# Kernel tuning notes

Hardware: AMD Instinct MI355X
Metric: run time of the kernel (lower is better)

The kernel has to match this reference:

```python
import jax, jax.numpy as jnp
import numpy as np
import math

B, N, D, H, K = 32, 512, 768, 12, 8  # batch, patches, hidden_dim, heads, n_topic_groups
HD = D // H


def setup_inputs() -> dict:
    key = jax.random.key(0)
    ks = jax.random.split(key, 12)
    hidden_states = jax.random.normal(ks[0], (B, N, D), jnp.float32)
    # group ids in 1..K, every group present (required by original sorted-dict indexing)
    tid = jax.random.permutation(ks[1], (jnp.arange(B, dtype=jnp.int64) % K) + 1)
    s = 1.0 / math.sqrt(D)
    def lin(k):
        kw, kb = jax.random.split(k)
        return (jax.random.normal(kw, (D, D), jnp.float32) * s,
                jax.random.normal(kb, (D,), jnp.float32) * s)
    Wq, bq = lin(ks[2])
    Wk, bk = lin(ks[3])
    Wv, bv = lin(ks[4])
    Wo, bo = lin(ks[5])
    Wc, bc = lin(ks[6])  # Conv1d(D, D, kernel_size=1) == pointwise linear
    return dict(hidden_states=hidden_states, tid=tid, Wq=Wq, bq=bq, Wk=Wk, bk=bk,
                Wv=Wv, bv=bv, Wo=Wo, bo=bo, Wc=Wc, bc=bc)


def reference(hidden_states, tid, Wq, bq, Wk, bk, Wv, bv, Wo, bo, Wc, bc):
    # --- context(): per-group context_aware + mean, scattered back ---
    # context_aware(x) = mean over group of (x + conv1x1(x)); conv is pointwise so
    # it commutes with grouping -> compute per-sample then segment-mean.
    y = hidden_states + jnp.einsum('bnd,ed->bne', hidden_states, Wc) + bc  # [B,N,D]
    seg = tid - 1  # ids are 1..K
    sums = jax.ops.segment_sum(y, seg, num_segments=K)                      # [K,N,D]
    counts = jax.ops.segment_sum(jnp.ones((B,), y.dtype), seg, num_segments=K)
    means = sums / jnp.maximum(counts, 1.0)[:, None, None]
    contexts = means[seg] + hidden_states                                   # [B,N,D]

    # --- dual-stage attention (dropout rate 0 / eval mode) ---
    def heads(x):  # [B,N,D] -> [B,H,N,HD]
        return x.reshape(B, N, H, HD).transpose(0, 2, 1, 3)

    q = heads(hidden_states @ Wq.T + bq)
    t = heads(contexts @ Wq.T + bq)  # topic_states also passes through self.query
    k = heads(hidden_states @ Wk.T + bk)
    v = heads(hidden_states @ Wv.T + bv)

    scale = 1.0 / math.sqrt(HD)
    p1 = jax.nn.softmax(jnp.einsum('bhqd,bhkd->bhqk', t, k) * scale, axis=-1)
    v_t = jnp.einsum('bhqk,bhkd->bhqd', p1, v)
    p2 = jax.nn.softmax(jnp.einsum('bhqd,bhkd->bhqk', q, t) * scale, axis=-1)
    ctx = jnp.einsum('bhqk,bhkd->bhqd', p2, v_t)

    ctx = ctx.transpose(0, 2, 1, 3).reshape(B, N, D)
    return ctx @ Wo.T + bo
```

## Files before the change

kernel.cpp:

```cpp
#include <hip/hip_runtime.h>
#include <hip/hip_bf16.h>


typedef __bf16 bf16_t;
typedef __bf16 bf16x8 __attribute__((ext_vector_type(8)));
typedef __bf16 bf16x4 __attribute__((ext_vector_type(4)));
typedef float f32x4 __attribute__((ext_vector_type(4)));

#define B_ 32
#define N_ 512
#define D_ 768
#define H_ 12
#define HD_ 64
#define K_ 8
#define ND_ (N_ * D_)

__device__ __forceinline__ f32x4 mfma16(bf16x8 a, bf16x8 b, f32x4 c) {
  return __builtin_amdgcn_mfma_f32_16x16x32_bf16(a, b, c, 0, 0, 0);
}

__device__ __forceinline__ bf16x8 addv8(bf16x8 a, bf16x8 b) {
  bf16x8 o;
#pragma unroll
  for (int j = 0; j < 8; ++j) o[j] = (bf16_t)((float)a[j] + (float)b[j]);
  return o;
}

__device__ __forceinline__ int seg_of(const int* tid, int b) {
  const bool is64 = (tid[1] == 0);
  int v = is64 ? (int)((const long long*)tid)[b] : tid[b];
  return v - 1;
}

__global__ __launch_bounds__(256) void k_cvt(const float* __restrict__ in,
                                             bf16_t* __restrict__ out) {
  const size_t i = ((size_t)blockIdx.x * 256 + threadIdx.x) * 8;
  f32x4 a = *(const f32x4*)(in + i);
  f32x4 b = *(const f32x4*)(in + i + 4);
  bf16x8 o;
#pragma unroll
  for (int j = 0; j < 4; ++j) { o[j] = (bf16_t)a[j]; o[4 + j] = (bf16_t)b[j]; }
  *(bf16x8*)(out + i) = o;
}

__device__ __forceinline__ void gemm_core(const bf16_t* __restrict__ A,
                                          const bf16_t* __restrict__ Bw,
                                          char* smem, f32x4 (&acc)[4][4]) {
  const int t = threadIdx.x;
  const int lane = t & 63, w = t >> 6;
  const int quad = lane >> 4, l15 = lane & 15;
  const int r0 = t >> 2;
  const int c0e = (t & 3) * 8;
  const int mRow = (w >> 1) * 64, nCol = (w & 1) * 64;

  bf16x8 pa0 = *(const bf16x8*)(A + (size_t)r0 * D_ + c0e);
  bf16x8 pa1 = *(const bf16x8*)(A + (size_t)(r0 + 64) * D_ + c0e);
  bf16x8 pb0 = *(const bf16x8*)(Bw + (size_t)r0 * D_ + c0e);
  bf16x8 pb1 = *(const bf16x8*)(Bw + (size_t)(r0 + 64) * D_ + c0e);
  *(bf16x8*)(smem + t * 16) = pa0;
  *(bf16x8*)(smem + t * 16 + 4096) = pa1;
  *(bf16x8*)(smem + 8192 + t * 16) = pb0;
  *(bf16x8*)(smem + 8192 + t * 16 + 4096) = pb1;

  for (int kb = 0; kb < 24; ++kb) {
    __syncthreads();
    char* cur = smem + (kb & 1) * 16384;
    char* nxt = smem + ((kb + 1) & 1) * 16384;
    if (kb < 23) {
      const int k0 = (kb + 1) * 32;
      pa0 = *(const bf16x8*)(A + (size_t)r0 * D_ + k0 + c0e);
      pa1 = *(const bf16x8*)(A + (size_t)(r0 + 64) * D_ + k0 + c0e);
      pb0 = *(const bf16x8*)(Bw + (size_t)r0 * D_ + k0 + c0e);
      pb1 = *(const bf16x8*)(Bw + (size_t)(r0 + 64) * D_ + k0 + c0e);
    }
    bf16x8 af[4], bfr[4];
#pragma unroll
    for (int mt = 0; mt < 4; ++mt)
      af[mt] = *(const bf16x8*)(cur + (mRow + mt * 16 + l15) * 64 + quad * 16);
#pragma unroll
    for (int nt = 0; nt < 4; ++nt)
      bfr[nt] = *(const bf16x8*)(cur + 8192 + (nCol + nt * 16 + l15) * 64 +
                                 quad * 16);
#pragma unroll
    for (int mt = 0; mt < 4; ++mt)
#pragma unroll
      for (int nt = 0; nt < 4; ++nt)
        acc[mt][nt] = mfma16(af[mt], bfr[nt], acc[mt][nt]);
    if (kb < 23) {
      *(bf16x8*)(nxt + t * 16) = pa0;
      *(bf16x8*)(nxt + t * 16 + 4096) = pa1;
      *(bf16x8*)(nxt + 8192 + t * 16) = pb0;
      *(bf16x8*)(nxt + 8192 + t * 16 + 4096) = pb1;
    }
  }
}

__device__ __forceinline__ void zero_acc(f32x4 (&acc)[4][4]) {
  const f32x4 z = {0.f, 0.f, 0.f, 0.f};
#pragma unroll
  for (int a = 0; a < 4; ++a)
#pragma unroll
    for (int b = 0; b < 4; ++b) acc[a][b] = z;
}

__global__ __launch_bounds__(256) void k_gemm_qkv(
    const bf16_t* __restrict__ X, const bf16_t* __restrict__ Wq,
    const bf16_t* __restrict__ Wk, const bf16_t* __restrict__ Wv,
    const float* __restrict__ bq, const float* __restrict__ bk,
    const float* __restrict__ bv, bf16_t* __restrict__ Q,
    bf16_t* __restrict__ Kb, bf16_t* __restrict__ V) {
  __shared__ alignas(16) char smem[32768];
  const int wsel = blockIdx.x / 6, nb = blockIdx.x % 6;
  const bf16_t* W = wsel == 0 ? Wq : wsel == 1 ? Wk : Wv;
  const float* bias = wsel == 0 ? bq : wsel == 1 ? bk : bv;
  bf16_t* Out = wsel == 0 ? Q : wsel == 1 ? Kb : V;

  f32x4 acc[4][4];
  zero_acc(acc);
  gemm_core(X + (size_t)blockIdx.y * 128 * D_, W + (size_t)nb * 128 * D_, smem,
            acc);

  const int lane = threadIdx.x & 63, w = threadIdx.x >> 6;
  const int quad = lane >> 4, l15 = lane & 15;
  const int mbase = blockIdx.y * 128 + (w >> 1) * 64;
  const int nbase = nb * 128 + (w & 1) * 64;
#pragma unroll
  for (int nt = 0; nt < 4; ++nt) {
    const int col = nbase + nt * 16 + l15;
    const float bb = bias[col];
#pragma unroll
    for (int mt = 0; mt < 4; ++mt)
#pragma unroll
      for (int r = 0; r < 4; ++r) {
        const int row = mbase + mt * 16 + quad * 4 + r;
        Out[(size_t)row * D_ + col] = (bf16_t)(acc[mt][nt][r] + bb);
      }
  }
}

__global__ __launch_bounds__(256) void k_gemm_plain(
    const bf16_t* __restrict__ A, const bf16_t* __restrict__ W,
    const float* __restrict__ bias, const bf16_t* __restrict__ addA,
    void* __restrict__ Out, int outF32) {
  __shared__ alignas(16) char smem[32768];
  f32x4 acc[4][4];
  zero_acc(acc);
  gemm_core(A + (size_t)blockIdx.x * 128 * D_, W + (size_t)blockIdx.y * 128 * D_,
            smem, acc);
  const int lane = threadIdx.x & 63, w = threadIdx.x >> 6;
  const int quad = lane >> 4, l15 = lane & 15;
  const int mbase = blockIdx.x * 128 + (w >> 1) * 64;
  const int nbase = blockIdx.y * 128 + (w & 1) * 64;
#pragma unroll
  for (int nt = 0; nt < 4; ++nt) {
    const int col = nbase + nt * 16 + l15;
    const float bb = bias ? bias[col] : 0.f;
#pragma unroll
    for (int mt = 0; mt < 4; ++mt)
#pragma unroll
      for (int r = 0; r < 4; ++r) {
        const int row = mbase + mt * 16 + quad * 4 + r;
        float v = acc[mt][nt][r] + bb;
        if (addA) v += (float)addA[(size_t)row * D_ + col];
        const size_t oi = (size_t)row * D_ + col;
        if (outF32) ((float*)Out)[oi] = v;
        else ((bf16_t*)Out)[oi] = (bf16_t)v;
      }
  }
}

__global__ __launch_bounds__(256) void k_segmean(const float* __restrict__ X,
                                                 const int* __restrict__ tid,
                                                 bf16_t* __restrict__ M) {
  const size_t i = ((size_t)blockIdx.x * 256 + threadIdx.x) * 8;
  float acc[K_][8];
  float cnt[K_];
#pragma unroll
  for (int k = 0; k < K_; ++k) {
    cnt[k] = 0.f;
#pragma unroll
    for (int j = 0; j < 8; ++j) acc[k][j] = 0.f;
  }
  const bool is64 = (tid[1] == 0);
  for (int b = 0; b < B_; ++b) {
    const int s = (is64 ? (int)((const long long*)tid)[b] : tid[b]) - 1;
    const float* p = X + (size_t)b * ND_ + i;
    f32x4 y0 = *(const f32x4*)p;
    f32x4 y1 = *(const f32x4*)(p + 4);
#pragma unroll
    for (int k = 0; k < K_; ++k) {
      const float msk = (s == k) ? 1.f : 0.f;
      cnt[k] += msk;
#pragma unroll
      for (int j = 0; j < 4; ++j) {
        acc[k][j] += msk * y0[j];
        acc[k][4 + j] += msk * y1[j];
      }
    }
  }
#pragma unroll
  for (int k = 0; k < K_; ++k) {
    const float inv = 1.f / fmaxf(cnt[k], 1.f);
    bf16x8 o;
#pragma unroll
    for (int j = 0; j < 8; ++j) o[j] = (bf16_t)(acc[k][j] * inv);
    *(bf16x8*)(M + (size_t)k * ND_ + i) = o;
  }
}

__global__ __launch_bounds__(256) void k_attn(const bf16_t* __restrict__ Qp,
                                              const bf16_t* __restrict__ Kp,
                                              const bf16_t* __restrict__ Vp,
                                              const bf16_t* __restrict__ Madd,
                                              const int* __restrict__ tid,
                                              bf16_t* __restrict__ Op,
                                              int addq) {
  __shared__ alignas(16) __bf16 Kt[64][72];
  __shared__ alignas(16) __bf16 Vt[64][72];
  __shared__ alignas(16) __bf16 Pl[4][32][72];

  const int lane = threadIdx.x & 63, w = threadIdx.x >> 6;
  const int quad = lane >> 4, l15 = lane & 15;
  const int b = blockIdx.y / H_, h = blockIdx.y % H_;
  const int q0 = blockIdx.x * 128 + w * 32;
  const size_t base = (size_t)b * ND_ + h * HD_;
  const float C = 0.18033688011112042f;
  const int sg = seg_of(tid, b);
  const bf16_t* Mh = Madd + (size_t)sg * ND_ + h * HD_;

  bf16x8 aq[2][2];
#pragma unroll
  for (int mt = 0; mt < 2; ++mt)
#pragma unroll
    for (int ks = 0; ks < 2; ++ks) {
      const size_t off = (size_t)(q0 + mt * 16 + l15) * D_ + ks * 32 + quad * 8;
      bf16x8 q = *(const bf16x8*)(Qp + base + off);
      if (addq == 1) q = addv8(q, *(const bf16x8*)(Mh + off));
      aq[mt][ks] = q;
    }

  f32x4 O[2][4];
  float lacc[2][4];
  {
    const f32x4 z = {0.f, 0.f, 0.f, 0.f};
#pragma unroll
    for (int mt = 0; mt < 2; ++mt)
#pragma unroll
      for (int nt = 0; nt < 4; ++nt) O[mt][nt] = z;
#pragma unroll
    for (int mt = 0; mt < 2; ++mt)
#pragma unroll
      for (int r = 0; r < 4; ++r) lacc[mt][r] = 0.f;
  }

  const int sr = threadIdx.x >> 2, sc = threadIdx.x & 3;
  const int sig_sr = ((sr & 15) << 2) | (sr >> 4);

  bf16x8 kr[2], vr[2];
#pragma unroll
  for (int half = 0; half < 2; ++half) {
    const int cc = sc + half * 4;
    const size_t off = (size_t)sr * D_ + cc * 8;
    bf16x8 kv = *(const bf16x8*)(Kp + base + off);
    if (addq == 2) kv = addv8(kv, *(const bf16x8*)(Mh + off));
    kr[half] = kv;
    vr[half] = *(const bf16x8*)(Vp + base + off);
  }

  for (int c0 = 0; c0 < N_; c0 += 64) {
    __syncthreads();
#pragma unroll
    for (int half = 0; half < 2; ++half) {
      const int cc = sc + half * 4;
      *(bf16x8*)(&Kt[sr][cc * 8]) = kr[half];
#pragma unroll
      for (int j = 0; j < 8; ++j) Vt[cc * 8 + j][sig_sr] = vr[half][j];
    }
    __syncthreads();

    if (c0 + 64 < N_) {
#pragma unroll
      for (int half = 0; half < 2; ++half) {
        const int cc = sc + half * 4;
        const size_t off = (size_t)(c0 + 64 + sr) * D_ + cc * 8;
        bf16x8 kv = *(const bf16x8*)(Kp + base + off);
        if (addq == 2) kv = addv8(kv, *(const bf16x8*)(Mh + off));
        kr[half] = kv;
        vr[half] = *(const bf16x8*)(Vp + base + off);
      }
    }

    f32x4 S[2][4];
    {
      const f32x4 z = {0.f, 0.f, 0.f, 0.f};
#pragma unroll
      for (int mt = 0; mt < 2; ++mt)
#pragma unroll
        for (int nt = 0; nt < 4; ++nt) S[mt][nt] = z;
    }
#pragma unroll
    for (int ks = 0; ks < 2; ++ks) {
      bf16x8 bk[4];
#pragma unroll
      for (int nt = 0; nt < 4; ++nt)
        bk[nt] = *(const bf16x8*)(&Kt[nt * 16 + l15][ks * 32 + quad * 8]);
#pragma unroll
      for (int mt = 0; mt < 2; ++mt)
#pragma unroll
        for (int nt = 0; nt < 4; ++nt)
          S[mt][nt] = mfma16(aq[mt][ks], bk[nt], S[mt][nt]);
    }

#pragma unroll
    for (int mt = 0; mt < 2; ++mt)
#pragma unroll
      for (int r = 0; r < 4; ++r) {
        bf16x4 pk;
#pragma unroll
        for (int nt = 0; nt < 4; ++nt) {
          const float p = exp2f(S[mt][nt][r] * C);
          lacc[mt][r] += p;
          pk[nt] = (bf16_t)p;
        }
        *(bf16x4*)(&Pl[w][mt * 16 + quad * 4 + r][l15 * 4]) = pk;
      }

#pragma unroll
    for (int ks2 = 0; ks2 < 2; ++ks2) {
      bf16x8 ap[2], bv[4];
#pragma unroll
      for (int mt = 0; mt < 2; ++mt)
        ap[mt] = *(const bf16x8*)(&Pl[w][mt * 16 + l15][ks2 * 32 + quad * 8]);
#pragma unroll
      for (int nt2 = 0; nt2 < 4; ++nt2)
        bv[nt2] = *(const bf16x8*)(&Vt[nt2 * 16 + l15][ks2 * 32 + quad * 8]);
#pragma unroll
      for (int mt = 0; mt < 2; ++mt)
#pragma unroll
        for (int nt2 = 0; nt2 < 4; ++nt2)
          O[mt][nt2] = mfma16(ap[mt], bv[nt2], O[mt][nt2]);
    }
  }

#pragma unroll
  for (int mt = 0; mt < 2; ++mt)
#pragma unroll
    for (int r = 0; r < 4; ++r) {
      float l = lacc[mt][r];
#pragma unroll
      for (int d = 1; d < 16; d <<= 1) l += __shfl_xor(l, d);
      const float inv = 1.f / l;
      const size_t row = base + (size_t)(q0 + mt * 16 + quad * 4 + r) * D_;
#pragma unroll
      for (int nt2 = 0; nt2 < 4; ++nt2)
        Op[row + nt2 * 16 + l15] = (bf16_t)(O[mt][nt2][r] * inv);
    }
}

__global__ __launch_bounds__(256) void k_zero(float* __restrict__ out) {
  const size_t i = ((size_t)blockIdx.x * 256 + threadIdx.x) * 8;
  f32x4 z = {0.f, 0.f, 0.f, 0.f};
  *(f32x4*)(out + i) = z;
  *(f32x4*)(out + i + 4) = z;
}

extern "C" void kernel_launch(void* const* d_in, const int* in_sizes, int n_in,
                              void* d_out, int out_size, void* d_ws,
                              size_t ws_size, hipStream_t stream) {
  const float* x  = (const float*)d_in[0];
  const int*  tid = (const int*)d_in[1];
  const float* Wq = (const float*)d_in[2];
  const float* bq = (const float*)d_in[3];
  const float* Wk = (const float*)d_in[4];
  const float* bk = (const float*)d_in[5];
  const float* Wv = (const float*)d_in[6];
  const float* bv = (const float*)d_in[7];
  const float* Wo = (const float*)d_in[8];
  const float* bo = (const float*)d_in[9];
  const float* Wc = (const float*)d_in[10];
  const float* bc = (const float*)d_in[11];

  const size_t SZ  = (size_t)B_ * ND_ * sizeof(bf16_t);
  const size_t MSZ = (size_t)K_ * ND_ * sizeof(bf16_t);
  const size_t WSZ = (size_t)D_ * D_ * sizeof(bf16_t);
  if (ws_size < 3 * SZ + MSZ + 5 * WSZ) {
    k_zero<<<6144, 256, 0, stream>>>((float*)d_out);
    return;
  }

  char* ws = (char*)d_ws;
  bf16_t* Qb  = (bf16_t*)(ws);
  bf16_t* Kb  = (bf16_t*)(ws + SZ);
  bf16_t* Vb  = (bf16_t*)(ws + 2 * SZ);
  bf16_t* Mq  = (bf16_t*)(ws + 3 * SZ);
  bf16_t* Wqb = (bf16_t*)(ws + 3 * SZ + MSZ);
  bf16_t* Wkb = (bf16_t*)(ws + 3 * SZ + MSZ + WSZ);
  bf16_t* Wvb = (bf16_t*)(ws + 3 * SZ + MSZ + 2 * WSZ);
  bf16_t* Wcb = (bf16_t*)(ws + 3 * SZ + MSZ + 3 * WSZ);
  bf16_t* Wob = (bf16_t*)(ws + 3 * SZ + MSZ + 4 * WSZ);
  bf16_t* Mx = Qb;
  bf16_t* Mb = Kb;
  bf16_t* VT = (bf16_t*)d_out;
  bf16_t* Xb = (bf16_t*)d_out + (size_t)B_ * ND_;
  bf16_t* CTX = Kb;

  k_cvt<<<6144, 256, 0, stream>>>(x, Xb);
  k_cvt<<<288, 256, 0, stream>>>(Wq, Wqb);
  k_cvt<<<288, 256, 0, stream>>>(Wk, Wkb);
  k_cvt<<<288, 256, 0, stream>>>(Wv, Wvb);
  k_cvt<<<288, 256, 0, stream>>>(Wc, Wcb);
  k_cvt<<<288, 256, 0, stream>>>(Wo, Wob);
  k_segmean<<<192, 256, 0, stream>>>(x, tid, Mx);
  k_gemm_plain<<<dim3(32, 6), 256, 0, stream>>>(Mx, Wcb, bc, Mx, Mb, 0);
  k_gemm_plain<<<dim3(32, 6), 256, 0, stream>>>(Mb, Wqb, nullptr, nullptr, Mq, 0);
  k_gemm_qkv<<<dim3(18, 128), 256, 0, stream>>>(Xb, Wqb, Wkb, Wvb, bq, bk, bv,
                                                Qb, Kb, Vb);
  k_attn<<<dim3(4, B_ * H_), 256, 0, stream>>>(Qb, Kb, Vb, Mq, tid, VT, 1);
  k_attn<<<dim3(4, B_ * H_), 256, 0, stream>>>(Qb, Qb, VT, Mq, tid, CTX, 2);
  k_gemm_plain<<<dim3(128, 6), 256, 0, stream>>>(CTX, Wob, bo, nullptr, d_out, 1);
}
```

Measured before the change: 434.4 us.

## XOR-swizzle GEMM LDS tiles, remap blocks across XCDs, merge convert launches

The shared-memory tile layout in the GEMM core gets an XOR swizzle on the 16-byte k-chunk index, so the per-lane fragment reads no longer hit the same LDS banks. The QKV and output-projection GEMMs now take a flattened 1D grid, remapped so that blocks on the same XCD (bid & 7) share row blocks, which improves L2 reuse of the A operand. The six separate fp32-to-bf16 conversion launches are merged into a single kernel to cut launch overhead. The trade-off is a little extra index arithmetic in each kernel.

Result: faster. 424.1 us (-2.4%).

```diff
diff --git a/kernel.cpp b/kernel.cpp
--- a/kernel.cpp
+++ b/kernel.cpp
@@ -32,9 +32,25 @@
   return v - 1;
 }
 
-__global__ __launch_bounds__(256) void k_cvt(const float* __restrict__ in,
-                                             bf16_t* __restrict__ out) {
-  const size_t i = ((size_t)blockIdx.x * 256 + threadIdx.x) * 8;
+__global__ __launch_bounds__(256) void k_cvt_all(
+    const float* __restrict__ x, const float* __restrict__ Wq,
+    const float* __restrict__ Wk, const float* __restrict__ Wv,
+    const float* __restrict__ Wc, const float* __restrict__ Wo,
+    bf16_t* __restrict__ Xb, bf16_t* __restrict__ Wqb,
+    bf16_t* __restrict__ Wkb, bf16_t* __restrict__ Wvb,
+    bf16_t* __restrict__ Wcb, bf16_t* __restrict__ Wob) {
+  int bid = blockIdx.x;
+  const float* in;
+  bf16_t* out;
+  if (bid < 6144) {
+    in = x; out = Xb;
+  } else {
+    const int wi = (bid - 6144) / 288;
+    bid = (bid - 6144) % 288;
+    in = wi == 0 ? Wq : wi == 1 ? Wk : wi == 2 ? Wv : wi == 3 ? Wc : Wo;
+    out = wi == 0 ? Wqb : wi == 1 ? Wkb : wi == 2 ? Wvb : wi == 3 ? Wcb : Wob;
+  }
+  const size_t i = ((size_t)bid * 256 + threadIdx.x) * 8;
   f32x4 a = *(const f32x4*)(in + i);
   f32x4 b = *(const f32x4*)(in + i + 4);
   bf16x8 o;
@@ -51,16 +67,20 @@
   const int quad = lane >> 4, l15 = lane & 15;
   const int r0 = t >> 2;
   const int c0e = (t & 3) * 8;
+  const int kcw = (t & 3) ^ ((r0 >> 1) & 3);
+  const int wo0 = r0 * 64 + kcw * 16;
+  const int wo1 = (r0 + 64) * 64 + kcw * 16;
+  const int kcr = quad ^ ((l15 >> 1) & 3);
   const int mRow = (w >> 1) * 64, nCol = (w & 1) * 64;
 
   bf16x8 pa0 = *(const bf16x8*)(A + (size_t)r0 * D_ + c0e);
   bf16x8 pa1 = *(const bf16x8*)(A + (size_t)(r0 + 64) * D_ + c0e);
   bf16x8 pb0 = *(const bf16x8*)(Bw + (size_t)r0 * D_ + c0e);
   bf16x8 pb1 = *(const bf16x8*)(Bw + (size_t)(r0 + 64) * D_ + c0e);
-  *(bf16x8*)(smem + t * 16) = pa0;
-  *(bf16x8*)(smem + t * 16 + 4096) = pa1;
-  *(bf16x8*)(smem + 8192 + t * 16) = pb0;
-  *(bf16x8*)(smem + 8192 + t * 16 + 4096) = pb1;
+  *(bf16x8*)(smem + wo0) = pa0;
+  *(bf16x8*)(smem + wo1) = pa1;
+  *(bf16x8*)(smem + 8192 + wo0) = pb0;
+  *(bf16x8*)(smem + 8192 + wo1) = pb1;
 
   for (int kb = 0; kb < 24; ++kb) {
     __syncthreads();
@@ -76,21 +96,21 @@
     bf16x8 af[4], bfr[4];
 #pragma unroll
     for (int mt = 0; mt < 4; ++mt)
-      af[mt] = *(const bf16x8*)(cur + (mRow + mt * 16 + l15) * 64 + quad * 16);
+      af[mt] = *(const bf16x8*)(cur + (mRow + mt * 16 + l15) * 64 + kcr * 16);
 #pragma unroll
     for (int nt = 0; nt < 4; ++nt)
       bfr[nt] = *(const bf16x8*)(cur + 8192 + (nCol + nt * 16 + l15) * 64 +
-                                 quad * 16);
+                                 kcr * 16);
 #pragma unroll
     for (int mt = 0; mt < 4; ++mt)
 #pragma unroll
       for (int nt = 0; nt < 4; ++nt)
         acc[mt][nt] = mfma16(af[mt], bfr[nt], acc[mt][nt]);
     if (kb < 23) {
-      *(bf16x8*)(nxt + t * 16) = pa0;
-      *(bf16x8*)(nxt + t * 16 + 4096) = pa1;
-      *(bf16x8*)(nxt + 8192 + t * 16) = pb0;
-      *(bf16x8*)(nxt + 8192 + t * 16 + 4096) = pb1;
+      *(bf16x8*)(nxt + wo0) = pa0;
+      *(bf16x8*)(nxt + wo1) = pa1;
+      *(bf16x8*)(nxt + 8192 + wo0) = pb0;
+      *(bf16x8*)(nxt + 8192 + wo1) = pb1;
     }
   }
 }
@@ -110,19 +130,22 @@
     const float* __restrict__ bv, bf16_t* __restrict__ Q,
     bf16_t* __restrict__ Kb, bf16_t* __restrict__ V) {
   __shared__ alignas(16) char smem[32768];
-  const int wsel = blockIdx.x / 6, nb = blockIdx.x % 6;
+  const int bid = blockIdx.x;
+  const int xcd = bid & 7, i = bid >> 3;
+  const int tile = i % 18, rowblk = (i / 18) * 8 + xcd;
+  const int wsel = tile / 6, nb = tile % 6;
   const bf16_t* W = wsel == 0 ? Wq : wsel == 1 ? Wk : Wv;
   const float* bias = wsel == 0 ? bq : wsel == 1 ? bk : bv;
   bf16_t* Out = wsel == 0 ? Q : wsel == 1 ? Kb : V;
 
   f32x4 acc[4][4];
   zero_acc(acc);
-  gemm_core(X + (size_t)blockIdx.y * 128 * D_, W + (size_t)nb * 128 * D_, smem,
+  gemm_core(X + (size_t)rowblk * 128 * D_, W + (size_t)nb * 128 * D_, smem,
             acc);
 
   const int lane = threadIdx.x & 63, w = threadIdx.x >> 6;
   const int quad = lane >> 4, l15 = lane & 15;
-  const int mbase = blockIdx.y * 128 + (w >> 1) * 64;
+  const int mbase = rowblk * 128 + (w >> 1) * 64;
   const int nbase = nb * 128 + (w & 1) * 64;
 #pragma unroll
   for (int nt = 0; nt < 4; ++nt) {
@@ -141,16 +164,26 @@
 __global__ __launch_bounds__(256) void k_gemm_plain(
     const bf16_t* __restrict__ A, const bf16_t* __restrict__ W,
     const float* __restrict__ bias, const bf16_t* __restrict__ addA,
-    void* __restrict__ Out, int outF32) {
+    void* __restrict__ Out, int outF32, int swz) {
   __shared__ alignas(16) char smem[32768];
+  int mblk, nblk;
+  if (swz) {
+    const int bid = blockIdx.x;
+    const int xcd = bid & 7, i = bid >> 3;
+    nblk = i % 6;
+    mblk = (i / 6) * 8 + xcd;
+  } else {
+    mblk = blockIdx.x;
+    nblk = blockIdx.y;
+  }
   f32x4 acc[4][4];
   zero_acc(acc);
-  gemm_core(A + (size_t)blockIdx.x * 128 * D_, W + (size_t)blockIdx.y * 128 * D_,
-            smem, acc);
+  gemm_core(A + (size_t)mblk * 128 * D_, W + (size_t)nblk * 128 * D_, smem,
+            acc);
   const int lane = threadIdx.x & 63, w = threadIdx.x >> 6;
   const int quad = lane >> 4, l15 = lane & 15;
-  const int mbase = blockIdx.x * 128 + (w >> 1) * 64;
-  const int nbase = blockIdx.y * 128 + (w & 1) * 64;
+  const int mbase = mblk * 128 + (w >> 1) * 64;
+  const int nbase = nblk * 128 + (w & 1) * 64;
 #pragma unroll
   for (int nt = 0; nt < 4; ++nt) {
     const int col = nbase + nt * 16 + l15;
@@ -404,18 +437,15 @@
   bf16_t* Xb = (bf16_t*)d_out + (size_t)B_ * ND_;
   bf16_t* CTX = Kb;
 
-  k_cvt<<<6144, 256, 0, stream>>>(x, Xb);
-  k_cvt<<<288, 256, 0, stream>>>(Wq, Wqb);
-  k_cvt<<<288, 256, 0, stream>>>(Wk, Wkb);
-  k_cvt<<<288, 256, 0, stream>>>(Wv, Wvb);
-  k_cvt<<<288, 256, 0, stream>>>(Wc, Wcb);
-  k_cvt<<<288, 256, 0, stream>>>(Wo, Wob);
+  k_cvt_all<<<7584, 256, 0, stream>>>(x, Wq, Wk, Wv, Wc, Wo, Xb, Wqb, Wkb,
+                                      Wvb, Wcb, Wob);
   k_segmean<<<192, 256, 0, stream>>>(x, tid, Mx);
-  k_gemm_plain<<<dim3(32, 6), 256, 0, stream>>>(Mx, Wcb, bc, Mx, Mb, 0);
-  k_gemm_plain<<<dim3(32, 6), 256, 0, stream>>>(Mb, Wqb, nullptr, nullptr, Mq, 0);
-  k_gemm_qkv<<<dim3(18, 128), 256, 0, stream>>>(Xb, Wqb, Wkb, Wvb, bq, bk, bv,
-                                                Qb, Kb, Vb);
+  k_gemm_plain<<<dim3(32, 6), 256, 0, stream>>>(Mx, Wcb, bc, Mx, Mb, 0, 0);
+  k_gemm_plain<<<dim3(32, 6), 256, 0, stream>>>(Mb, Wqb, nullptr, nullptr, Mq,
+                                                0, 0);
+  k_gemm_qkv<<<2304, 256, 0, stream>>>(Xb, Wqb, Wkb, Wvb, bq, bk, bv, Qb, Kb,
+                                       Vb);
   k_attn<<<dim3(4, B_ * H_), 256, 0, stream>>>(Qb, Kb, Vb, Mq, tid, VT, 1);
   k_attn<<<dim3(4, B_ * H_), 256, 0, stream>>>(Qb, Qb, VT, Mq, tid, CTX, 2);
-  k_gemm_plain<<<dim3(128, 6), 256, 0, stream>>>(CTX, Wob, bo, nullptr, d_out, 1);
-}
+  k_gemm_plain<<<768, 256, 0, stream>>>(CTX, Wob, bo, nullptr, d_out, 1, 1);
+}
```
